# Kernel optimization log

Measured on AMD Instinct MI355X. Metric: run time of the kernel, lower is better.

## Reference

```python
import jax, jax.numpy as jnp
import numpy as np

VARIANCE = (0.1, 0.2)
THRESHOLD = 0.5
NEG_POS = 3


def point_form(boxes):
    # (cx,cy,w,h) -> (xmin,ymin,xmax,ymax)
    return jnp.concatenate([boxes[:, :2] - boxes[:, 2:] / 2,
                            boxes[:, :2] + boxes[:, 2:] / 2], axis=1)


def jaccard(a, b):
    # a: [T,4] xyxy truths, b: [P,4] xyxy priors -> IoU [T,P]
    lt = jnp.maximum(a[:, None, :2], b[None, :, :2])
    rb = jnp.minimum(a[:, None, 2:], b[None, :, 2:])
    wh = jnp.clip(rb - lt, 0.0)
    inter = wh[..., 0] * wh[..., 1]
    area_a = ((a[:, 2] - a[:, 0]) * (a[:, 3] - a[:, 1]))[:, None]
    area_b = ((b[:, 2] - b[:, 0]) * (b[:, 3] - b[:, 1]))[None, :]
    return inter / (area_a + area_b - inter)


def encode(matched, priors):
    g_cxcy = (matched[:, :2] + matched[:, 2:]) / 2 - priors[:, :2]
    g_cxcy = g_cxcy / (VARIANCE[0] * priors[:, 2:])
    g_wh = jnp.log((matched[:, 2:] - matched[:, :2]) / priors[:, 2:]) / VARIANCE[1]
    return jnp.concatenate([g_cxcy, g_wh], axis=1)


def match_one(truths, priors):
    # SSD match for one image; labels are zeroed in BiBoxLoss -> binary conf {0,1}
    overlaps = jaccard(truths, point_form(priors))          # [T,P]
    best_prior_idx = jnp.argmax(overlaps, axis=1)           # [T]
    best_truth_overlap = jnp.max(overlaps, axis=0)          # [P]
    best_truth_idx = jnp.argmax(overlaps, axis=0)           # [P]
    best_truth_overlap = best_truth_overlap.at[best_prior_idx].set(2.0)
    best_truth_idx = best_truth_idx.at[best_prior_idx].set(
        jnp.arange(truths.shape[0]))
    matched = truths[best_truth_idx]                        # [P,4]
    conf = jnp.where(best_truth_overlap < THRESHOLD, 0, 1)  # [P] int
    loc = encode(matched, priors)
    return loc, conf


def bibox_loss(loc_data, conf_data, priors, targets):
    num, num_priors = loc_data.shape[0], loc_data.shape[1]
    truths = targets[..., :4]                               # [B,T,4]
    loc_t, conf_t = jax.vmap(lambda t: match_one(t, priors))(truths)

    pos = conf_t > 0                                        # [B,P]
    # smooth L1 (sum) over positive priors
    ad = jnp.abs(loc_data - loc_t)
    sl1 = jnp.where(ad < 1.0, 0.5 * ad * ad, ad - 0.5)
    loss_l = jnp.sum(sl1 * pos[..., None].astype(loc_data.dtype))

    # per-prior CE (logsumexp - gathered logit) for hard-negative mining
    lse = jax.nn.logsumexp(conf_data, axis=-1)              # [B,P]
    gathered = jnp.take_along_axis(conf_data, conf_t[..., None], axis=-1)[..., 0]
    loss_c_all = lse - gathered                             # [B,P]

    loss_c_mine = jnp.where(pos, 0.0, loss_c_all)
    loss_idx = jnp.argsort(-loss_c_mine, axis=1)
    idx_rank = jnp.argsort(loss_idx, axis=1)                # rank of each prior
    num_pos = jnp.sum(pos.astype(jnp.int32), axis=1, keepdims=True)  # [B,1]
    num_neg = jnp.minimum(NEG_POS * num_pos, num_priors - 1)
    neg = idx_rank < num_neg                                # [B,P]

    sel = pos | neg
    loss_c = jnp.sum(jnp.where(sel, loss_c_all, 0.0))

    N = jnp.sum(num_pos).astype(loc_data.dtype)
    return loss_l / N, loss_c / N


def setup_inputs() -> dict:
    key = jax.random.key(0)
    k1, k2, k3, k4, k5, k6 = jax.random.split(key, 6)
    B, P, T = 32, 65536, 16
    loc_data = jax.random.normal(k1, (B, P, 4), dtype=jnp.float32)
    conf_data = jax.random.normal(k2, (B, P, 2), dtype=jnp.float32)
    # priors: valid center-form boxes
    pc = 0.15 + 0.7 * jax.random.uniform(k3, (P, 2), dtype=jnp.float32)
    pwh = 0.05 + 0.25 * jax.random.uniform(k4, (P, 2), dtype=jnp.float32)
    priors = jnp.concatenate([pc, pwh], axis=1)
    # targets: valid corner-form boxes + dummy label column (zeroed by the loss)
    tc = 0.2 + 0.6 * jax.random.uniform(k5, (B, T, 2), dtype=jnp.float32)
    twh = 0.05 + 0.25 * jax.random.uniform(k6, (B, T, 2), dtype=jnp.float32)
    boxes = jnp.concatenate([tc - twh / 2, tc + twh / 2], axis=-1)
    targets = jnp.concatenate(
        [boxes, jnp.ones((B, T, 1), dtype=jnp.float32)], axis=-1)
    return {"loc_data": loc_data, "conf_data": conf_data,
            "priors": priors, "targets": targets}


def reference(loc_data, conf_data, priors, targets):
    return bibox_loss(loc_data, conf_data, priors, targets)
```

## Files before the change

kernel.cpp:

```cpp
#include <hip/hip_runtime.h>

#define NB_ 32
#define NP_ 65536
#define NT_ 16
#define HB 1024
#define HSCALE 128.0f

__device__ __forceinline__ unsigned long long shfl_down_u64(unsigned long long v, int off) {
    unsigned lo = (unsigned)(v & 0xffffffffULL);
    unsigned hi = (unsigned)(v >> 32);
    lo = __shfl_down(lo, off, 64);
    hi = __shfl_down(hi, off, 64);
    return (((unsigned long long)hi) << 32) | (unsigned long long)lo;
}

__device__ __forceinline__ float softplus_(float x) {
    return fmaxf(x, 0.0f) + __logf(1.0f + __expf(-fabsf(x)));
}

__device__ __forceinline__ float iou_fast(float tx0, float ty0, float tx1, float ty1, float ta,
                                          float bx0, float by0, float bx1, float by1, float ar) {
    float lx = fmaxf(tx0, bx0), ly = fmaxf(ty0, by0);
    float rx = fminf(tx1, bx1), ry = fminf(ty1, by1);
    float w = fmaxf(rx - lx, 0.0f), h = fmaxf(ry - ly, 0.0f);
    float inter = w * h;
    return __fdividef(inter, ta + ar - inter);
}

__global__ void __launch_bounds__(256) fusedAC(
    const float* __restrict__ loc, const float* __restrict__ conf,
    const float* __restrict__ priors, const float* __restrict__ targets,
    unsigned long long* __restrict__ bestPrior, int* __restrict__ num_pos,
    float* __restrict__ sums_ll, float* __restrict__ sums_pc,
    int* __restrict__ hcnt, float* __restrict__ hsum)
{
    int b = blockIdx.y;
    __shared__ float tr[NT_][5];
    __shared__ int hc[HB];
    __shared__ float hs[HB];
    __shared__ unsigned long long shb[4][NT_];
    __shared__ float sh_ll[4], sh_pc[4];
    __shared__ int sh_np[4];

    int tid = threadIdx.x;
    for (int i = tid; i < HB; i += 256) { hc[i] = 0; hs[i] = 0.0f; }
    if (tid < NT_) {
        const float* tp = targets + ((size_t)b * NT_ + tid) * 5;
        float x0 = tp[0], y0 = tp[1], x1 = tp[2], y1 = tp[3];
        tr[tid][0] = x0; tr[tid][1] = y0; tr[tid][2] = x1; tr[tid][3] = y1;
        tr[tid][4] = (x1 - x0) * (y1 - y0);
    }
    __syncthreads();

    int p0 = blockIdx.x * 1024 + tid;
    float bx0[4], by0[4], bx1[4], by1[4], ar[4];
#pragma unroll
    for (int i = 0; i < 4; i++) {
        float4 pr = ((const float4*)priors)[p0 + 256 * i];
        float hw = pr.z * 0.5f, hh = pr.w * 0.5f;
        bx0[i] = pr.x - hw; by0[i] = pr.y - hh;
        bx1[i] = pr.x + hw; by1[i] = pr.y + hh;
        ar[i] = (bx1[i] - bx0[i]) * (by1[i] - by0[i]);
    }
    float bestI[4] = {-1.f, -1.f, -1.f, -1.f};
    int bestT[4] = {0, 0, 0, 0};
    unsigned long long best[NT_];
#pragma unroll
    for (int t = 0; t < NT_; t++) best[t] = 0ULL;

#pragma unroll
    for (int t = 0; t < NT_; t++) {
        float tx0 = tr[t][0], ty0 = tr[t][1], tx1 = tr[t][2], ty1 = tr[t][3], ta = tr[t][4];
        float mi = -1.0f; int pi = 0;
#pragma unroll
        for (int i = 0; i < 4; i++) {
            float iou = iou_fast(tx0, ty0, tx1, ty1, ta, bx0[i], by0[i], bx1[i], by1[i], ar[i]);
            if (iou > bestI[i]) { bestI[i] = iou; bestT[i] = t; }
            if (iou > mi) { mi = iou; pi = i; }
        }
        unsigned long long pk = (((unsigned long long)__float_as_uint(mi)) << 32)
                              | (unsigned)(~(p0 + 256 * pi));
        if (pk > best[t]) best[t] = pk;
    }

    float ll_acc = 0.0f, pc_acc = 0.0f;
    int np_acc = 0;
#pragma unroll
    for (int i = 0; i < 4; i++) {
        int p = p0 + 256 * i;
        size_t bp = (size_t)b * NP_ + p;
        bool pos = !(bestI[i] < 0.5f);
        float2 c = ((const float2*)conf)[bp];
        float d = c.y - c.x;
        float v = pos ? 0.0f : softplus_(d);
        int bin = min(HB - 1, (int)(v * HSCALE));
        atomicAdd(&hc[bin], 1);
        atomicAdd(&hs[bin], v);
        if (pos) {
            np_acc++;
            pc_acc += softplus_(-d);
            int t = bestT[i];
            float tx0 = tr[t][0], ty0 = tr[t][1], tx1 = tr[t][2], ty1 = tr[t][3];
            float4 pr = ((const float4*)priors)[p];
            float gcx = ((tx0 + tx1) * 0.5f - pr.x) / (0.1f * pr.z);
            float gcy = ((ty0 + ty1) * 0.5f - pr.y) / (0.1f * pr.w);
            float gw = __logf((tx1 - tx0) / pr.z) * 5.0f;
            float gh = __logf((ty1 - ty0) / pr.w) * 5.0f;
            float4 ld = ((const float4*)loc)[bp];
            float d0 = fabsf(ld.x - gcx), d1 = fabsf(ld.y - gcy);
            float d2 = fabsf(ld.z - gw),  d3 = fabsf(ld.w - gh);
            ll_acc += (d0 < 1.0f) ? 0.5f * d0 * d0 : d0 - 0.5f;
            ll_acc += (d1 < 1.0f) ? 0.5f * d1 * d1 : d1 - 0.5f;
            ll_acc += (d2 < 1.0f) ? 0.5f * d2 * d2 : d2 - 0.5f;
            ll_acc += (d3 < 1.0f) ? 0.5f * d3 * d3 : d3 - 0.5f;
        }
    }

    int wave = tid >> 6, lane = tid & 63;
#pragma unroll
    for (int t = 0; t < NT_; t++) {
        unsigned long long v = best[t];
        for (int off = 32; off > 0; off >>= 1) {
            unsigned long long u = shfl_down_u64(v, off);
            if (u > v) v = u;
        }
        if (lane == 0) shb[wave][t] = v;
    }
    for (int off = 32; off > 0; off >>= 1) {
        ll_acc += __shfl_down(ll_acc, off, 64);
        pc_acc += __shfl_down(pc_acc, off, 64);
        np_acc += __shfl_down(np_acc, off, 64);
    }
    if (lane == 0) { sh_ll[wave] = ll_acc; sh_pc[wave] = pc_acc; sh_np[wave] = np_acc; }
    __syncthreads();

    if (tid < NT_) {
        unsigned long long v = shb[0][tid];
        for (int w = 1; w < 4; w++) { unsigned long long u = shb[w][tid]; if (u > v) v = u; }
        atomicMax(&bestPrior[b * NT_ + tid], v);
    }
    if (tid == 0) {
        float a = sh_ll[0] + sh_ll[1] + sh_ll[2] + sh_ll[3];
        float c2 = sh_pc[0] + sh_pc[1] + sh_pc[2] + sh_pc[3];
        int n = sh_np[0] + sh_np[1] + sh_np[2] + sh_np[3];
        if (a != 0.0f) atomicAdd(&sums_ll[b], a);
        if (c2 != 0.0f) atomicAdd(&sums_pc[b], c2);
        if (n) atomicAdd(&num_pos[b], n);
    }
    for (int i = tid; i < HB; i += 256) {
        int c = hc[i];
        if (c) {
            atomicAdd(&hcnt[b * HB + i], c);
            atomicAdd(&hsum[b * HB + i], hs[i]);
        }
    }
}

__global__ void fixup(const float* __restrict__ loc, const float* __restrict__ conf,
                      const float* __restrict__ priors, const float* __restrict__ targets,
                      const unsigned long long* __restrict__ bestPrior,
                      int* __restrict__ num_pos, float* __restrict__ sums_ll,
                      float* __restrict__ sums_pc, int* __restrict__ hcnt,
                      float* __restrict__ hsum)
{
    int b = blockIdx.x;
    int t = threadIdx.x;
    __shared__ unsigned ps[NT_];
    __shared__ float tr[NT_][4];
    __shared__ float ta[NT_];
    if (t < NT_) {
        ps[t] = ~((unsigned)(bestPrior[b * NT_ + t] & 0xffffffffULL));
        const float* tp = targets + ((size_t)b * NT_ + t) * 5;
        tr[t][0] = tp[0]; tr[t][1] = tp[1]; tr[t][2] = tp[2]; tr[t][3] = tp[3];
        ta[t] = (tp[2] - tp[0]) * (tp[3] - tp[1]);
    }
    __syncthreads();
    if (t >= NT_) return;
    unsigned p = ps[t];
    for (int u = t + 1; u < NT_; u++)
        if (ps[u] == p) return;

    float4 pr = ((const float4*)priors)[p];
    float hw = pr.z * 0.5f, hh = pr.w * 0.5f;
    float bx0 = pr.x - hw, by0 = pr.y - hh;
    float bx1 = pr.x + hw, by1 = pr.y + hh;
    float areab = (bx1 - bx0) * (by1 - by0);
    float bestI = -1.0f;
    int t0 = 0;
#pragma unroll
    for (int tt = 0; tt < NT_; tt++) {
        float iou = iou_fast(tr[tt][0], tr[tt][1], tr[tt][2], tr[tt][3], ta[tt],
                             bx0, by0, bx1, by1, areab);
        if (iou > bestI) { bestI = iou; t0 = tt; }
    }
    bool pos0 = !(bestI < 0.5f);

    size_t bp = (size_t)b * NP_ + p;
    float2 c = ((const float2*)conf)[bp];
    float d = c.y - c.x;
    float4 ld = ((const float4*)loc)[bp];

    auto sl1_of = [&](int tt) -> float {
        float tx0 = tr[tt][0], ty0 = tr[tt][1], tx1 = tr[tt][2], ty1 = tr[tt][3];
        float gcx = ((tx0 + tx1) * 0.5f - pr.x) / (0.1f * pr.z);
        float gcy = ((ty0 + ty1) * 0.5f - pr.y) / (0.1f * pr.w);
        float gw = __logf((tx1 - tx0) / pr.z) * 5.0f;
        float gh = __logf((ty1 - ty0) / pr.w) * 5.0f;
        float d0 = fabsf(ld.x - gcx), d1 = fabsf(ld.y - gcy);
        float d2 = fabsf(ld.z - gw),  d3 = fabsf(ld.w - gh);
        float s = (d0 < 1.0f) ? 0.5f * d0 * d0 : d0 - 0.5f;
        s += (d1 < 1.0f) ? 0.5f * d1 * d1 : d1 - 0.5f;
        s += (d2 < 1.0f) ? 0.5f * d2 * d2 : d2 - 0.5f;
        s += (d3 < 1.0f) ? 0.5f * d3 * d3 : d3 - 0.5f;
        return s;
    };

    float dll = sl1_of(t) - (pos0 ? sl1_of(t0) : 0.0f);
    if (dll != 0.0f) atomicAdd(&sums_ll[b], dll);
    if (!pos0) {
        float v = softplus_(d);
        int bin = min(HB - 1, (int)(v * HSCALE));
        atomicSub(&hcnt[b * HB + bin], 1);
        atomicAdd(&hsum[b * HB + bin], -v);
        atomicAdd(&sums_pc[b], softplus_(-d));
        atomicAdd(&num_pos[b], 1);
    }
}

__global__ void __launch_bounds__(256) selectD2(const int* __restrict__ hcnt,
                                                const float* __restrict__ hsum,
                                                const int* __restrict__ num_pos,
                                                float* __restrict__ topk) {
    int b = blockIdx.x;
    __shared__ int cnt[HB];
    __shared__ float sm[HB];
    __shared__ unsigned ccnt[16];
    __shared__ float csm[16];
    int tid = threadIdx.x;
    for (int i = tid; i < HB; i += 256) {
        cnt[i] = hcnt[b * HB + i];
        sm[i] = hsum[b * HB + i];
    }
    __syncthreads();
    if (tid < 16) {
        unsigned c = 0; float s = 0.0f;
        for (int j = 0; j < 64; j++) { c += (unsigned)cnt[tid * 64 + j]; s += sm[tid * 64 + j]; }
        ccnt[tid] = c; csm[tid] = s;
    }
    __syncthreads();
    if (tid == 0) {
        int K = 3 * num_pos[b];
        if (K > NP_ - 1) K = NP_ - 1;
        float tk = 0.0f;
        if (K > 0) {
            unsigned need = (unsigned)K, cum = 0;
            float s = 0.0f;
            int cb = 15;
            for (; cb > 0; --cb) {
                if (cum + ccnt[cb] >= need) break;
                cum += ccnt[cb]; s += csm[cb];
            }
            int bin = cb * 64 + 63;
            for (; bin > cb * 64; --bin) {
                if (cum + (unsigned)cnt[bin] >= need) break;
                cum += (unsigned)cnt[bin]; s += sm[bin];
            }
            unsigned rem = need - cum;
            int c = cnt[bin];
            float avg = (c > 0) ? __fdividef(sm[bin], (float)c) : 0.0f;
            tk = s + (float)rem * avg;
        }
        topk[b] = tk;
    }
}

__global__ void finalD4(const int* __restrict__ num_pos, const float* __restrict__ sums_ll,
                        const float* __restrict__ sums_pc, const float* __restrict__ topk,
                        float* __restrict__ out) {
    int t = threadIdx.x;
    float ll = 0.0f, pc = 0.0f, tk = 0.0f;
    int n = 0;
    if (t < NB_) { ll = sums_ll[t]; pc = sums_pc[t]; tk = topk[t]; n = num_pos[t]; }
    for (int off = 32; off > 0; off >>= 1) {
        ll += __shfl_down(ll, off, 64);
        pc += __shfl_down(pc, off, 64);
        tk += __shfl_down(tk, off, 64);
        n  += __shfl_down(n, off, 64);
    }
    if (t == 0) {
        float fn = (float)n;
        out[0] = ll / fn;
        out[1] = (pc + tk) / fn;
    }
}

extern "C" void kernel_launch(void* const* d_in, const int* in_sizes, int n_in,
                              void* d_out, int out_size, void* d_ws, size_t ws_size,
                              hipStream_t stream) {
    const float* loc = (const float*)d_in[0];
    const float* conf = (const float*)d_in[1];
    const float* priors = (const float*)d_in[2];
    const float* targets = (const float*)d_in[3];
    float* out = (float*)d_out;

    char* w = (char*)d_ws;
    int* hcnt = (int*)w;
    float* hsum = (float*)(w + (128u << 10));
    char* acc = w + (256u << 10);
    unsigned long long* bestPrior = (unsigned long long*)acc;
    int* num_pos = (int*)(acc + 4096);
    float* sums_ll = (float*)(acc + 4224);
    float* sums_pc = (float*)(acc + 4352);
    float* topk    = (float*)(acc + 4480);

    hipMemsetAsync(w, 0, (256u << 10) + 8192, stream);
    fusedAC<<<dim3(64, 32), 256, 0, stream>>>(loc, conf, priors, targets, bestPrior,
                                              num_pos, sums_ll, sums_pc, hcnt, hsum);
    fixup<<<NB_, 64, 0, stream>>>(loc, conf, priors, targets, bestPrior,
                                  num_pos, sums_ll, sums_pc, hcnt, hsum);
    selectD2<<<NB_, 256, 0, stream>>>(hcnt, hsum, num_pos, topk);
    finalD4<<<1, 64, 0, stream>>>(num_pos, sums_ll, sums_pc, topk, out);
}
```

Baseline: 164.8 us.

## Replace atomics and memset with per-block partials and fuse tail kernels

The main kernel now handles four 1024-prior chunks per block, so the grid shrinks to 16 blocks per image. It writes per-block histograms, partial sums and best-prior keys to workspace instead of using global atomics, and it packs IoU and index into 32-bit keys with a ballot-based argmax. The fixup, select and final kernels are merged into one finish kernel that reduces the partials and uses a ticket counter for the last-block global reduction. This removes the memset and two launches, in exchange for fewer blocks (512), lower occupancy, and a truncated-IoU tie-break that can differ from exact argmax.

New measurement: 242.9 us. 1.47x slower.

```diff
diff --git a/kernel.cpp b/kernel.cpp
--- a/kernel.cpp
+++ b/kernel.cpp
@@ -5,14 +5,8 @@
 #define NT_ 16
 #define HB 1024
 #define HSCALE 128.0f
-
-__device__ __forceinline__ unsigned long long shfl_down_u64(unsigned long long v, int off) {
-    unsigned lo = (unsigned)(v & 0xffffffffULL);
-    unsigned hi = (unsigned)(v >> 32);
-    lo = __shfl_down(lo, off, 64);
-    hi = __shfl_down(hi, off, 64);
-    return (((unsigned long long)hi) << 32) | (unsigned long long)lo;
-}
+#define NBX 16
+#define CHUNKS 4
 
 __device__ __forceinline__ float softplus_(float x) {
     return fmaxf(x, 0.0f) + __logf(1.0f + __expf(-fabsf(x)));
@@ -27,22 +21,25 @@
     return __fdividef(inter, ta + ar - inter);
 }
 
-__global__ void __launch_bounds__(256) fusedAC(
+__global__ void __launch_bounds__(256, 4) mainK(
     const float* __restrict__ loc, const float* __restrict__ conf,
     const float* __restrict__ priors, const float* __restrict__ targets,
-    unsigned long long* __restrict__ bestPrior, int* __restrict__ num_pos,
-    float* __restrict__ sums_ll, float* __restrict__ sums_pc,
-    int* __restrict__ hcnt, float* __restrict__ hsum)
+    int* __restrict__ gcnt, float* __restrict__ gsum,
+    unsigned long long* __restrict__ bestPart,
+    float* __restrict__ part_ll, float* __restrict__ part_pc, int* __restrict__ part_np,
+    unsigned* __restrict__ ticket)
 {
-    int b = blockIdx.y;
+    const int bx = blockIdx.x, b = blockIdx.y, tid = threadIdx.x;
+
     __shared__ float tr[NT_][5];
     __shared__ int hc[HB];
     __shared__ float hs[HB];
-    __shared__ unsigned long long shb[4][NT_];
+    __shared__ unsigned wkey[4][NT_], wp[4][NT_];
     __shared__ float sh_ll[4], sh_pc[4];
     __shared__ int sh_np[4];
 
-    int tid = threadIdx.x;
+    if (b == 0 && bx == 0 && tid == 0) *ticket = 0u;
+
     for (int i = tid; i < HB; i += 256) { hc[i] = 0; hs[i] = 0.0f; }
     if (tid < NT_) {
         const float* tp = targets + ((size_t)b * NT_ + tid) * 5;
@@ -52,79 +49,89 @@
     }
     __syncthreads();
 
-    int p0 = blockIdx.x * 1024 + tid;
-    float bx0[4], by0[4], bx1[4], by1[4], ar[4];
-#pragma unroll
-    for (int i = 0; i < 4; i++) {
-        float4 pr = ((const float4*)priors)[p0 + 256 * i];
-        float hw = pr.z * 0.5f, hh = pr.w * 0.5f;
-        bx0[i] = pr.x - hw; by0[i] = pr.y - hh;
-        bx1[i] = pr.x + hw; by1[i] = pr.y + hh;
-        ar[i] = (bx1[i] - bx0[i]) * (by1[i] - by0[i]);
-    }
-    float bestI[4] = {-1.f, -1.f, -1.f, -1.f};
-    int bestT[4] = {0, 0, 0, 0};
-    unsigned long long best[NT_];
-#pragma unroll
-    for (int t = 0; t < NT_; t++) best[t] = 0ULL;
-
-#pragma unroll
-    for (int t = 0; t < NT_; t++) {
-        float tx0 = tr[t][0], ty0 = tr[t][1], tx1 = tr[t][2], ty1 = tr[t][3], ta = tr[t][4];
-        float mi = -1.0f; int pi = 0;
-#pragma unroll
-        for (int i = 0; i < 4; i++) {
-            float iou = iou_fast(tx0, ty0, tx1, ty1, ta, bx0[i], by0[i], bx1[i], by1[i], ar[i]);
-            if (iou > bestI[i]) { bestI[i] = iou; bestT[i] = t; }
-            if (iou > mi) { mi = iou; pi = i; }
-        }
-        unsigned long long pk = (((unsigned long long)__float_as_uint(mi)) << 32)
-                              | (unsigned)(~(p0 + 256 * pi));
-        if (pk > best[t]) best[t] = pk;
-    }
-
     float ll_acc = 0.0f, pc_acc = 0.0f;
     int np_acc = 0;
-#pragma unroll
-    for (int i = 0; i < 4; i++) {
-        int p = p0 + 256 * i;
-        size_t bp = (size_t)b * NP_ + p;
-        bool pos = !(bestI[i] < 0.5f);
-        float2 c = ((const float2*)conf)[bp];
-        float d = c.y - c.x;
-        float v = pos ? 0.0f : softplus_(d);
-        int bin = min(HB - 1, (int)(v * HSCALE));
-        atomicAdd(&hc[bin], 1);
-        atomicAdd(&hs[bin], v);
-        if (pos) {
-            np_acc++;
-            pc_acc += softplus_(-d);
-            int t = bestT[i];
-            float tx0 = tr[t][0], ty0 = tr[t][1], tx1 = tr[t][2], ty1 = tr[t][3];
-            float4 pr = ((const float4*)priors)[p];
-            float gcx = ((tx0 + tx1) * 0.5f - pr.x) / (0.1f * pr.z);
-            float gcy = ((ty0 + ty1) * 0.5f - pr.y) / (0.1f * pr.w);
-            float gw = __logf((tx1 - tx0) / pr.z) * 5.0f;
-            float gh = __logf((ty1 - ty0) / pr.w) * 5.0f;
-            float4 ld = ((const float4*)loc)[bp];
-            float d0 = fabsf(ld.x - gcx), d1 = fabsf(ld.y - gcy);
-            float d2 = fabsf(ld.z - gw),  d3 = fabsf(ld.w - gh);
-            ll_acc += (d0 < 1.0f) ? 0.5f * d0 * d0 : d0 - 0.5f;
-            ll_acc += (d1 < 1.0f) ? 0.5f * d1 * d1 : d1 - 0.5f;
-            ll_acc += (d2 < 1.0f) ? 0.5f * d2 * d2 : d2 - 0.5f;
-            ll_acc += (d3 < 1.0f) ? 0.5f * d3 * d3 : d3 - 0.5f;
-        }
-    }
-
-    int wave = tid >> 6, lane = tid & 63;
+    unsigned tkey[NT_];
+#pragma unroll
+    for (int t = 0; t < NT_; t++) tkey[t] = 0u;
+
+    for (int c = 0; c < CHUNKS; c++) {
+        const int pbase = (bx * CHUNKS + c) * 1024 + tid;
+        float4 pr[4];
+        float pbx0[4], pby0[4], pbx1[4], pby1[4], par[4];
+#pragma unroll
+        for (int i = 0; i < 4; i++) {
+            pr[i] = ((const float4*)priors)[pbase + 256 * i];
+            float hw = pr[i].z * 0.5f, hh = pr[i].w * 0.5f;
+            pbx0[i] = pr[i].x - hw; pby0[i] = pr[i].y - hh;
+            pbx1[i] = pr[i].x + hw; pby1[i] = pr[i].y + hh;
+            par[i] = (pbx1[i] - pbx0[i]) * (pby1[i] - pby0[i]);
+        }
+        unsigned pkey[4] = {0u, 0u, 0u, 0u};
+#pragma unroll
+        for (int t = 0; t < NT_; t++) {
+            float tx0 = tr[t][0], ty0 = tr[t][1], tx1 = tr[t][2], ty1 = tr[t][3], ta = tr[t][4];
+            unsigned lowt = (unsigned)(15 - t);
+            unsigned lowc = (unsigned)(15 - c * 4);
+#pragma unroll
+            for (int i = 0; i < 4; i++) {
+                float iou = iou_fast(tx0, ty0, tx1, ty1, ta,
+                                     pbx0[i], pby0[i], pbx1[i], pby1[i], par[i]);
+                unsigned base = (__float_as_uint(iou) & 0xFFFFFFFCu) << 2;
+                unsigned kt = base | lowt;
+                unsigned kp = base | (lowc - (unsigned)i);
+                pkey[i] = (kt > pkey[i]) ? kt : pkey[i];
+                tkey[t] = (kp > tkey[t]) ? kp : tkey[t];
+            }
+        }
+#pragma unroll
+        for (int i = 0; i < 4; i++) {
+            int p = pbase + 256 * i;
+            size_t bp = (size_t)b * NP_ + p;
+            bool pos = (pkey[i] >= 0xFC000000u);
+            float2 cxy = ((const float2*)conf)[bp];
+            float dd = cxy.y - cxy.x;
+            float v = pos ? 0.0f : softplus_(dd);
+            int bin = min(HB - 1, (int)(v * HSCALE));
+            atomicAdd(&hc[bin], 1);
+            atomicAdd(&hs[bin], v);
+            if (pos) {
+                np_acc++;
+                pc_acc += softplus_(-dd);
+                int t = 15 - (int)(pkey[i] & 15u);
+                float tx0 = tr[t][0], ty0 = tr[t][1], tx1 = tr[t][2], ty1 = tr[t][3];
+                float gcx = ((tx0 + tx1) * 0.5f - pr[i].x) / (0.1f * pr[i].z);
+                float gcy = ((ty0 + ty1) * 0.5f - pr[i].y) / (0.1f * pr[i].w);
+                float gw = __logf((tx1 - tx0) / pr[i].z) * 5.0f;
+                float gh = __logf((ty1 - ty0) / pr[i].w) * 5.0f;
+                float4 ld = ((const float4*)loc)[bp];
+                float d0 = fabsf(ld.x - gcx), d1 = fabsf(ld.y - gcy);
+                float d2 = fabsf(ld.z - gw),  d3 = fabsf(ld.w - gh);
+                ll_acc += (d0 < 1.0f) ? 0.5f * d0 * d0 : d0 - 0.5f;
+                ll_acc += (d1 < 1.0f) ? 0.5f * d1 * d1 : d1 - 0.5f;
+                ll_acc += (d2 < 1.0f) ? 0.5f * d2 * d2 : d2 - 0.5f;
+                ll_acc += (d3 < 1.0f) ? 0.5f * d3 * d3 : d3 - 0.5f;
+            }
+        }
+    }
+
+    const int wave = tid >> 6, lane = tid & 63;
 #pragma unroll
     for (int t = 0; t < NT_; t++) {
-        unsigned long long v = best[t];
+        unsigned k = tkey[t], m = k;
         for (int off = 32; off > 0; off >>= 1) {
-            unsigned long long u = shfl_down_u64(v, off);
-            if (u > v) v = u;
-        }
-        if (lane == 0) shb[wave][t] = v;
+            unsigned o = __shfl_down(m, off, 64);
+            m = (o > m) ? o : m;
+        }
+        m = __shfl(m, 0, 64);
+        unsigned long long ball = __ballot(k == m);
+        if (lane == 0) {
+            int l = __ffsll((long long)ball) - 1;
+            int ci = 15 - (int)(m & 15u);
+            int p = bx * (CHUNKS * 1024) + ci * 256 + wave * 64 + l;
+            wkey[wave][t] = m;
+            wp[wave][t] = (unsigned)p;
+        }
     }
     for (int off = 32; off > 0; off >>= 1) {
         ll_acc += __shfl_down(ll_acc, off, 64);
@@ -135,121 +142,140 @@
     __syncthreads();
 
     if (tid < NT_) {
-        unsigned long long v = shb[0][tid];
-        for (int w = 1; w < 4; w++) { unsigned long long u = shb[w][tid]; if (u > v) v = u; }
-        atomicMax(&bestPrior[b * NT_ + tid], v);
+        unsigned bk = wkey[0][tid], bpv = wp[0][tid];
+        for (int w = 1; w < 4; w++) {
+            unsigned k2 = wkey[w][tid], p2 = wp[w][tid];
+            if (k2 > bk || (k2 == bk && p2 < bpv)) { bk = k2; bpv = p2; }
+        }
+        unsigned long long pk = (((unsigned long long)bk) << 32) | (unsigned)(~bpv);
+        bestPart[((size_t)b * NT_ + tid) * NBX + bx] = pk;
     }
     if (tid == 0) {
-        float a = sh_ll[0] + sh_ll[1] + sh_ll[2] + sh_ll[3];
-        float c2 = sh_pc[0] + sh_pc[1] + sh_pc[2] + sh_pc[3];
-        int n = sh_np[0] + sh_np[1] + sh_np[2] + sh_np[3];
-        if (a != 0.0f) atomicAdd(&sums_ll[b], a);
-        if (c2 != 0.0f) atomicAdd(&sums_pc[b], c2);
-        if (n) atomicAdd(&num_pos[b], n);
-    }
-    for (int i = tid; i < HB; i += 256) {
-        int c = hc[i];
-        if (c) {
-            atomicAdd(&hcnt[b * HB + i], c);
-            atomicAdd(&hsum[b * HB + i], hs[i]);
-        }
-    }
-}
-
-__global__ void fixup(const float* __restrict__ loc, const float* __restrict__ conf,
-                      const float* __restrict__ priors, const float* __restrict__ targets,
-                      const unsigned long long* __restrict__ bestPrior,
-                      int* __restrict__ num_pos, float* __restrict__ sums_ll,
-                      float* __restrict__ sums_pc, int* __restrict__ hcnt,
-                      float* __restrict__ hsum)
+        part_ll[b * NBX + bx] = sh_ll[0] + sh_ll[1] + sh_ll[2] + sh_ll[3];
+        part_pc[b * NBX + bx] = sh_pc[0] + sh_pc[1] + sh_pc[2] + sh_pc[3];
+        part_np[b * NBX + bx] = sh_np[0] + sh_np[1] + sh_np[2] + sh_np[3];
+    }
+    int* gc = gcnt + ((size_t)(b * NBX + bx)) * HB;
+    float* gs = gsum + ((size_t)(b * NBX + bx)) * HB;
+    for (int i = tid; i < HB; i += 256) { gc[i] = hc[i]; gs[i] = hs[i]; }
+}
+
+__global__ void __launch_bounds__(256) finishK(
+    const float* __restrict__ loc, const float* __restrict__ conf,
+    const float* __restrict__ priors, const float* __restrict__ targets,
+    const int* __restrict__ gcnt, const float* __restrict__ gsum,
+    const unsigned long long* __restrict__ bestPart,
+    const float* __restrict__ part_ll, const float* __restrict__ part_pc,
+    const int* __restrict__ part_np,
+    float* __restrict__ final_l, float* __restrict__ final_c, int* __restrict__ final_n,
+    unsigned* __restrict__ ticket, float* __restrict__ out)
 {
-    int b = blockIdx.x;
-    int t = threadIdx.x;
+    const int b = blockIdx.x, tid = threadIdx.x;
+    __shared__ int hc[HB];
+    __shared__ float hs[HB];
+    __shared__ float tr[NT_][5];
     __shared__ unsigned ps[NT_];
-    __shared__ float tr[NT_][4];
-    __shared__ float ta[NT_];
-    if (t < NT_) {
-        ps[t] = ~((unsigned)(bestPrior[b * NT_ + t] & 0xffffffffULL));
-        const float* tp = targets + ((size_t)b * NT_ + t) * 5;
-        tr[t][0] = tp[0]; tr[t][1] = tp[1]; tr[t][2] = tp[2]; tr[t][3] = tp[3];
-        ta[t] = (tp[2] - tp[0]) * (tp[3] - tp[1]);
-    }
-    __syncthreads();
-    if (t >= NT_) return;
-    unsigned p = ps[t];
-    for (int u = t + 1; u < NT_; u++)
-        if (ps[u] == p) return;
-
-    float4 pr = ((const float4*)priors)[p];
-    float hw = pr.z * 0.5f, hh = pr.w * 0.5f;
-    float bx0 = pr.x - hw, by0 = pr.y - hh;
-    float bx1 = pr.x + hw, by1 = pr.y + hh;
-    float areab = (bx1 - bx0) * (by1 - by0);
-    float bestI = -1.0f;
-    int t0 = 0;
-#pragma unroll
-    for (int tt = 0; tt < NT_; tt++) {
-        float iou = iou_fast(tr[tt][0], tr[tt][1], tr[tt][2], tr[tt][3], ta[tt],
-                             bx0, by0, bx1, by1, areab);
-        if (iou > bestI) { bestI = iou; t0 = tt; }
-    }
-    bool pos0 = !(bestI < 0.5f);
-
-    size_t bp = (size_t)b * NP_ + p;
-    float2 c = ((const float2*)conf)[bp];
-    float d = c.y - c.x;
-    float4 ld = ((const float4*)loc)[bp];
-
-    auto sl1_of = [&](int tt) -> float {
-        float tx0 = tr[tt][0], ty0 = tr[tt][1], tx1 = tr[tt][2], ty1 = tr[tt][3];
-        float gcx = ((tx0 + tx1) * 0.5f - pr.x) / (0.1f * pr.z);
-        float gcy = ((ty0 + ty1) * 0.5f - pr.y) / (0.1f * pr.w);
-        float gw = __logf((tx1 - tx0) / pr.z) * 5.0f;
-        float gh = __logf((ty1 - ty0) / pr.w) * 5.0f;
-        float d0 = fabsf(ld.x - gcx), d1 = fabsf(ld.y - gcy);
-        float d2 = fabsf(ld.z - gw),  d3 = fabsf(ld.w - gh);
-        float s = (d0 < 1.0f) ? 0.5f * d0 * d0 : d0 - 0.5f;
-        s += (d1 < 1.0f) ? 0.5f * d1 * d1 : d1 - 0.5f;
-        s += (d2 < 1.0f) ? 0.5f * d2 * d2 : d2 - 0.5f;
-        s += (d3 < 1.0f) ? 0.5f * d3 * d3 : d3 - 0.5f;
-        return s;
-    };
-
-    float dll = sl1_of(t) - (pos0 ? sl1_of(t0) : 0.0f);
-    if (dll != 0.0f) atomicAdd(&sums_ll[b], dll);
-    if (!pos0) {
-        float v = softplus_(d);
-        int bin = min(HB - 1, (int)(v * HSCALE));
-        atomicSub(&hcnt[b * HB + bin], 1);
-        atomicAdd(&hsum[b * HB + bin], -v);
-        atomicAdd(&sums_pc[b], softplus_(-d));
-        atomicAdd(&num_pos[b], 1);
-    }
-}
-
-__global__ void __launch_bounds__(256) selectD2(const int* __restrict__ hcnt,
-                                                const float* __restrict__ hsum,
-                                                const int* __restrict__ num_pos,
-                                                float* __restrict__ topk) {
-    int b = blockIdx.x;
-    __shared__ int cnt[HB];
-    __shared__ float sm[HB];
+    __shared__ float s_dll, s_dpc;
+    __shared__ int s_dnp;
     __shared__ unsigned ccnt[16];
     __shared__ float csm[16];
-    int tid = threadIdx.x;
+    __shared__ int s_last;
+
+    if (tid == 0) { s_dll = 0.0f; s_dpc = 0.0f; s_dnp = 0; s_last = 0; }
+    if (tid < NT_) {
+        const float* tp = targets + ((size_t)b * NT_ + tid) * 5;
+        float x0 = tp[0], y0 = tp[1], x1 = tp[2], y1 = tp[3];
+        tr[tid][0] = x0; tr[tid][1] = y0; tr[tid][2] = x1; tr[tid][3] = y1;
+        tr[tid][4] = (x1 - x0) * (y1 - y0);
+    }
     for (int i = tid; i < HB; i += 256) {
-        cnt[i] = hcnt[b * HB + i];
-        sm[i] = hsum[b * HB + i];
-    }
-    __syncthreads();
+        int c = 0; float s = 0.0f;
+        for (int j = 0; j < NBX; j++) {
+            c += gcnt[((size_t)(b * NBX + j)) * HB + i];
+            s += gsum[((size_t)(b * NBX + j)) * HB + i];
+        }
+        hc[i] = c; hs[i] = s;
+    }
+    if (tid < NT_) {
+        unsigned long long v = bestPart[((size_t)b * NT_ + tid) * NBX];
+        for (int j = 1; j < NBX; j++) {
+            unsigned long long u = bestPart[((size_t)b * NT_ + tid) * NBX + j];
+            if (u > v) v = u;
+        }
+        ps[tid] = ~((unsigned)(v & 0xffffffffULL));
+    }
+    __syncthreads();
+
+    if (tid < NT_) {
+        unsigned p = ps[tid];
+        bool active = true;
+        for (int u = tid + 1; u < NT_; u++)
+            if (ps[u] == p) { active = false; break; }
+        if (active) {
+            float4 prv = ((const float4*)priors)[p];
+            float hw = prv.z * 0.5f, hh = prv.w * 0.5f;
+            float qx0 = prv.x - hw, qy0 = prv.y - hh;
+            float qx1 = prv.x + hw, qy1 = prv.y + hh;
+            float areab = (qx1 - qx0) * (qy1 - qy0);
+            unsigned pk = 0u;
+            for (int tt = 0; tt < NT_; tt++) {
+                float iou = iou_fast(tr[tt][0], tr[tt][1], tr[tt][2], tr[tt][3], tr[tt][4],
+                                     qx0, qy0, qx1, qy1, areab);
+                unsigned cand = ((__float_as_uint(iou) & 0xFFFFFFFCu) << 2)
+                              | (unsigned)(15 - tt);
+                pk = (cand > pk) ? cand : pk;
+            }
+            bool pos0 = (pk >= 0xFC000000u);
+            int t0 = 15 - (int)(pk & 15u);
+            size_t bp = (size_t)b * NP_ + p;
+            float2 cxy = ((const float2*)conf)[bp];
+            float dd = cxy.y - cxy.x;
+            float4 ld = ((const float4*)loc)[bp];
+
+            auto sl1_of = [&](int tt) -> float {
+                float tx0 = tr[tt][0], ty0 = tr[tt][1], tx1 = tr[tt][2], ty1 = tr[tt][3];
+                float gcx = ((tx0 + tx1) * 0.5f - prv.x) / (0.1f * prv.z);
+                float gcy = ((ty0 + ty1) * 0.5f - prv.y) / (0.1f * prv.w);
+                float gw = __logf((tx1 - tx0) / prv.z) * 5.0f;
+                float gh = __logf((ty1 - ty0) / prv.w) * 5.0f;
+                float d0 = fabsf(ld.x - gcx), d1 = fabsf(ld.y - gcy);
+                float d2 = fabsf(ld.z - gw),  d3 = fabsf(ld.w - gh);
+                float s = (d0 < 1.0f) ? 0.5f * d0 * d0 : d0 - 0.5f;
+                s += (d1 < 1.0f) ? 0.5f * d1 * d1 : d1 - 0.5f;
+                s += (d2 < 1.0f) ? 0.5f * d2 * d2 : d2 - 0.5f;
+                s += (d3 < 1.0f) ? 0.5f * d3 * d3 : d3 - 0.5f;
+                return s;
+            };
+            float dll = sl1_of(tid) - (pos0 ? sl1_of(t0) : 0.0f);
+            atomicAdd(&s_dll, dll);
+            if (!pos0) {
+                float v = softplus_(dd);
+                int bin = min(HB - 1, (int)(v * HSCALE));
+                atomicSub(&hc[bin], 1);
+                atomicAdd(&hs[bin], -v);
+                atomicAdd(&s_dpc, softplus_(-dd));
+                atomicAdd(&s_dnp, 1);
+            }
+        }
+    }
+    __syncthreads();
+
     if (tid < 16) {
-        unsigned c = 0; float s = 0.0f;
-        for (int j = 0; j < 64; j++) { c += (unsigned)cnt[tid * 64 + j]; s += sm[tid * 64 + j]; }
-        ccnt[tid] = c; csm[tid] = s;
-    }
-    __syncthreads();
+        unsigned cacc = 0; float sacc = 0.0f;
+        for (int j = 0; j < 64; j++) { cacc += (unsigned)hc[tid * 64 + j]; sacc += hs[tid * 64 + j]; }
+        ccnt[tid] = cacc; csm[tid] = sacc;
+    }
+    __syncthreads();
+
     if (tid == 0) {
-        int K = 3 * num_pos[b];
+        float sll = s_dll, spc = s_dpc;
+        int n = s_dnp;
+        for (int j = 0; j < NBX; j++) {
+            sll += part_ll[b * NBX + j];
+            spc += part_pc[b * NBX + j];
+            n += part_np[b * NBX + j];
+        }
+        int K = 3 * n;
         if (K > NP_ - 1) K = NP_ - 1;
         float tk = 0.0f;
         if (K > 0) {
@@ -262,35 +288,40 @@
             }
             int bin = cb * 64 + 63;
             for (; bin > cb * 64; --bin) {
-                if (cum + (unsigned)cnt[bin] >= need) break;
-                cum += (unsigned)cnt[bin]; s += sm[bin];
+                if (cum + (unsigned)hc[bin] >= need) break;
+                cum += (unsigned)hc[bin]; s += hs[bin];
             }
             unsigned rem = need - cum;
-            int c = cnt[bin];
-            float avg = (c > 0) ? __fdividef(sm[bin], (float)c) : 0.0f;
+            int cv = hc[bin];
+            float avg = (cv > 0) ? __fdividef(hs[bin], (float)cv) : 0.0f;
             tk = s + (float)rem * avg;
         }
-        topk[b] = tk;
-    }
-}
-
-__global__ void finalD4(const int* __restrict__ num_pos, const float* __restrict__ sums_ll,
-                        const float* __restrict__ sums_pc, const float* __restrict__ topk,
-                        float* __restrict__ out) {
-    int t = threadIdx.x;
-    float ll = 0.0f, pc = 0.0f, tk = 0.0f;
-    int n = 0;
-    if (t < NB_) { ll = sums_ll[t]; pc = sums_pc[t]; tk = topk[t]; n = num_pos[t]; }
-    for (int off = 32; off > 0; off >>= 1) {
-        ll += __shfl_down(ll, off, 64);
-        pc += __shfl_down(pc, off, 64);
-        tk += __shfl_down(tk, off, 64);
-        n  += __shfl_down(n, off, 64);
-    }
-    if (t == 0) {
-        float fn = (float)n;
-        out[0] = ll / fn;
-        out[1] = (pc + tk) / fn;
+        final_l[b] = sll;
+        final_c[b] = spc + tk;
+        final_n[b] = n;
+        __threadfence();
+        unsigned old = atomicAdd(ticket, 1u);
+        if (old == NB_ - 1) s_last = 1;
+    }
+    __syncthreads();
+
+    if (s_last) {
+        __threadfence();
+        if (tid < 64) {
+            float lv = 0.0f, cv = 0.0f;
+            int nv = 0;
+            if (tid < NB_) { lv = final_l[tid]; cv = final_c[tid]; nv = final_n[tid]; }
+            for (int off = 32; off > 0; off >>= 1) {
+                lv += __shfl_down(lv, off, 64);
+                cv += __shfl_down(cv, off, 64);
+                nv += __shfl_down(nv, off, 64);
+            }
+            if (tid == 0) {
+                float fn = (float)nv;
+                out[0] = lv / fn;
+                out[1] = cv / fn;
+            }
+        }
     }
 }
 
@@ -304,20 +335,22 @@
     float* out = (float*)d_out;
 
     char* w = (char*)d_ws;
-    int* hcnt = (int*)w;
-    float* hsum = (float*)(w + (128u << 10));
-    char* acc = w + (256u << 10);
-    unsigned long long* bestPrior = (unsigned long long*)acc;
-    int* num_pos = (int*)(acc + 4096);
-    float* sums_ll = (float*)(acc + 4224);
-    float* sums_pc = (float*)(acc + 4352);
-    float* topk    = (float*)(acc + 4480);
-
-    hipMemsetAsync(w, 0, (256u << 10) + 8192, stream);
-    fusedAC<<<dim3(64, 32), 256, 0, stream>>>(loc, conf, priors, targets, bestPrior,
-                                              num_pos, sums_ll, sums_pc, hcnt, hsum);
-    fixup<<<NB_, 64, 0, stream>>>(loc, conf, priors, targets, bestPrior,
-                                  num_pos, sums_ll, sums_pc, hcnt, hsum);
-    selectD2<<<NB_, 256, 0, stream>>>(hcnt, hsum, num_pos, topk);
-    finalD4<<<1, 64, 0, stream>>>(num_pos, sums_ll, sums_pc, topk, out);
-}
+    int* gcnt = (int*)w;
+    float* gsum = (float*)(w + (2u << 20));
+    char* acc = w + (4u << 20);
+    unsigned long long* bestPart = (unsigned long long*)acc;
+    float* part_ll = (float*)(acc + 65536);
+    float* part_pc = (float*)(acc + 65536 + 2048);
+    int* part_np   = (int*)(acc + 65536 + 4096);
+    float* final_l = (float*)(acc + 65536 + 6144);
+    float* final_c = (float*)(acc + 65536 + 6272);
+    int* final_n   = (int*)(acc + 65536 + 6400);
+    unsigned* ticket = (unsigned*)(acc + 65536 + 6528);
+
+    mainK<<<dim3(NBX, NB_), 256, 0, stream>>>(loc, conf, priors, targets,
+                                              gcnt, gsum, bestPart,
+                                              part_ll, part_pc, part_np, ticket);
+    finishK<<<NB_, 256, 0, stream>>>(loc, conf, priors, targets, gcnt, gsum, bestPart,
+                                     part_ll, part_pc, part_np,
+                                     final_l, final_c, final_n, ticket, out);
+}
```
